# Optimization experiments

Measured on AMD Instinct MI355X. Metric: run time of the kernel, lower is better.

The kernel has to match this reference:

```python
import jax, jax.numpy as jnp
import numpy as np


def setup_inputs() -> dict:
    key = jax.random.key(0)
    k1, k2, k3, k4 = jax.random.split(key, 4)
    B, S, IN, OUT = 4, 2048, 4096, 11008
    input = jax.random.normal(k1, (B, S, IN), dtype=jnp.float32)
    # int8-range quantized weights, stored as int32 (symmetric, zero_point = 0)
    int8_weights = jax.random.randint(k2, (OUT, IN), -128, 128, dtype=jnp.int32)
    scales = jax.random.normal(k3, (OUT,), dtype=jnp.float32)
    bias = jax.random.normal(k4, (1, OUT), dtype=jnp.float32)
    return {"input": input, "int8_weights": int8_weights, "scales": scales, "bias": bias}


def reference(input, int8_weights, scales, bias):
    # w8_a32_forward: dequantize per-output-channel (zero_point = 0) then linear.
    # out = input @ ((q_w * s_w[:, None]).T) + bias
    # Equivalent, cheaper form: scale the GEMM output per column instead of
    # materializing a second fp32 weight copy twice.
    w = int8_weights.astype(jnp.float32)            # [OUT, IN]
    acc = jnp.einsum('bsi,oi->bso', input, w)        # [B, S, OUT]
    return acc * scales + bias                       # broadcast over [B, S, OUT]
```

## Files before the change

kernel.cpp:

```cpp
#include <hip/hip_runtime.h>
#include <hip/hip_bf16.h>
#include <stdint.h>

typedef float f32x4 __attribute__((ext_vector_type(4)));
typedef int i32x4 __attribute__((ext_vector_type(4)));

__device__ __forceinline__ void gload_lds16(const signed char* g, signed char* l) {
    __builtin_amdgcn_global_load_lds(
        (const __attribute__((address_space(1))) unsigned int*)g,
        (__attribute__((address_space(3))) unsigned int*)l,
        16, 0, 0);
}

__global__ __launch_bounds__(256) void quant_rows_kernel(
        const float* __restrict__ A, signed char* __restrict__ Aq,
        float* __restrict__ qrow, int K) {
    const long row = blockIdx.x;
    const float* a = A + row * (long)K;
    signed char* o = Aq + row * (long)K;
    const int tid = threadIdx.x;
    const int nch = K >> 2;
    float amax = 0.f;
    for (int c = tid; c < nch; c += 256) {
        f32x4 v = ((const f32x4*)a)[c];
        amax = fmaxf(amax, fmaxf(fmaxf(fabsf(v[0]), fabsf(v[1])),
                                 fmaxf(fabsf(v[2]), fabsf(v[3]))));
    }
#pragma unroll
    for (int off = 32; off; off >>= 1)
        amax = fmaxf(amax, __shfl_xor(amax, off, 64));
    __shared__ float red[4];
    if ((tid & 63) == 0) red[tid >> 6] = amax;
    __syncthreads();
    amax = fmaxf(fmaxf(red[0], red[1]), fmaxf(red[2], red[3]));
    const float s = amax > 0.f ? 127.f / amax : 0.f;
    if (tid == 0) qrow[row] = amax > 0.f ? amax / 127.f : 0.f;
    for (int c = tid; c < nch; c += 256) {
        f32x4 v = ((const f32x4*)a)[c];
        int r = 0;
#pragma unroll
        for (int i = 0; i < 4; ++i) {
            int q = (int)__builtin_rintf(v[i] * s);
            r |= (q & 0xff) << (8 * i);
        }
        ((int*)o)[c] = r;
    }
}

__global__ __launch_bounds__(256) void cvt_i32_i8_kernel(
        const int* __restrict__ in, signed char* __restrict__ out, long n) {
    long base = ((long)blockIdx.x * 256 + threadIdx.x) * 16;
    long stride = (long)gridDim.x * 256 * 16;
    for (long i = base; i < n; i += stride) {
        i32x4 pk;
#pragma unroll
        for (int c = 0; c < 4; ++c) {
            i32x4 v = *(const i32x4*)(in + i + c * 4);
            pk[c] = (v[0] & 0xff) | ((v[1] & 0xff) << 8) |
                    ((v[2] & 0xff) << 16) | ((v[3] & 0xff) << 24);
        }
        *(i32x4*)(out + i) = pk;
    }
}


template<int BUF, int MH>
__device__ __forceinline__ void readAf(const signed char* smem, i32x4 (&fa)[4],
                                       const int (&off)[4]) {
    const signed char* rg = smem + BUF * 32768 + MH * 8192;
#pragma unroll
    for (int ml = 0; ml < 4; ++ml)
        fa[ml] = *(const i32x4*)(rg + off[ml]);
}

template<int BUF, int NH>
__device__ __forceinline__ void readBf(const signed char* smem, i32x4 (&fb)[2],
                                       const int (&off)[2]) {
    const signed char* rg = smem + BUF * 32768 + 16384 + NH * 8192;
#pragma unroll
    for (int nl = 0; nl < 2; ++nl)
        fb[nl] = *(const i32x4*)(rg + off[nl]);
}

template<int MH, int NH>
__device__ __forceinline__ void mfmas(i32x4 (&acc)[8][4],
                                      const i32x4 (&fa)[4], const i32x4 (&fb)[2]) {
#pragma unroll
    for (int ml = 0; ml < 4; ++ml)
#pragma unroll
        for (int nl = 0; nl < 2; ++nl)
            acc[MH * 4 + ml][NH * 2 + nl] = __builtin_amdgcn_mfma_i32_16x16x64_i8(
                fa[ml], fb[nl], acc[MH * 4 + ml][NH * 2 + nl], 0, 0, 0);
}

#define BARw()  __builtin_amdgcn_s_barrier()
#define LG0()   { asm volatile("s_waitcnt lgkmcnt(0)" ::: "memory"); \
                  __builtin_amdgcn_sched_barrier(0); }
#define P1()    __builtin_amdgcn_s_setprio(1)
#define P0()    __builtin_amdgcn_s_setprio(0)
#define VM2()   asm volatile("s_waitcnt vmcnt(2)" ::: "memory")
#define VM0()   asm volatile("s_waitcnt vmcnt(0)" ::: "memory")

__global__ __launch_bounds__(512, 1) void gemm_i8_8phase(
        const signed char* __restrict__ A,
        const signed char* __restrict__ W,
        const float* __restrict__ qrow,
        const float* __restrict__ scales,
        const float* __restrict__ bias,
        float* __restrict__ C,
        int M, int N, int K) {
    extern __shared__ signed char smem[];

    const int tid  = threadIdx.x;
    const int lane = tid & 63;
    const int wid  = tid >> 6;
    const int wr = wid >> 2;
    const int wc = wid & 3;
    const int fr = lane & 15;
    const int fq = lane >> 4;
    const int kg = lane >> 4;

    const int nwg = gridDim.x;
    const int bid = blockIdx.x;
    const int swz = ((nwg & 7) == 0) ? ((bid & 7) * (nwg >> 3) + (bid >> 3)) : bid;
    const int tiles_n = N >> 8;
    const int tm = swz / tiles_n;
    const int tn = swz % tiles_n;
    const int arow = tm << 8;
    const int brow = tn << 8;

    int aRd[4], bRd[2];
#pragma unroll
    for (int ml = 0; ml < 4; ++ml) {
        const int lrow = wr * 16 + ml * 32 + fr;
        aRd[ml] = lrow * 64 + ((kg ^ ((lrow >> 1) & 3)) << 4);
    }
#pragma unroll
    for (int nl = 0; nl < 2; ++nl) {
        const int lrow = wc * 16 + nl * 64 + fr;
        bRd[nl] = lrow * 64 + ((kg ^ ((lrow >> 1) & 3)) << 4);
    }

    const int srow = tid >> 2;
    const int sswz = (((tid & 3) ^ ((srow >> 1) & 3)) << 4);
    int aOff[2], wOff[2];
#pragma unroll
    for (int h = 0; h < 2; ++h) {
        aOff[h] = (arow + h * 128 + srow) * K + sswz;
        wOff[h] = (brow + h * 128 + srow) * K + sswz;
    }
    const int ldsSt = wid * 1024;

#define STA(kt, h) gload_lds16(A + aOff[h] + (kt) * 64, \
                               smem + ((kt) & 1) * 32768 + (h) * 8192 + ldsSt)
#define STB(kt, h) gload_lds16(W + wOff[h] + (kt) * 64, \
                               smem + ((kt) & 1) * 32768 + 16384 + (h) * 8192 + ldsSt)

    i32x4 acc[8][4] = {};
    i32x4 faA[4], faB[4], fb0[2], fb1[2];

    const int NT = K >> 6;

    STA(0, 0); STB(0, 0); STA(0, 1); STB(0, 1);
    STA(1, 0); STB(1, 0); STB(1, 1);
    asm volatile("s_waitcnt vmcnt(3)" ::: "memory");
    BARw();
    readAf<0, 0>(smem, faA, aRd);
    readBf<0, 0>(smem, fb0, bRd);

    for (int i = 0; i < (NT >> 1) - 1; ++i) {
        const int b = 2 * i + 1, c = 2 * i + 2, d = 2 * i + 3;
        BARw(); LG0(); P1(); mfmas<0, 0>(acc, faA, fb0); P0();
        readBf<0, 1>(smem, fb1, bRd); STA(b, 1);
        BARw(); LG0(); P1(); mfmas<0, 1>(acc, faA, fb1); P0();
        readAf<0, 1>(smem, faB, aRd); STA(c, 0);
        BARw(); LG0(); P1(); mfmas<1, 0>(acc, faB, fb0); P0();
        STB(c, 0); VM2();
        BARw(); P1(); mfmas<1, 1>(acc, faB, fb1); P0();
        readAf<1, 0>(smem, faA, aRd); readBf<1, 0>(smem, fb0, bRd); STB(c, 1);
        BARw(); LG0(); P1(); mfmas<0, 0>(acc, faA, fb0); P0();
        readBf<1, 1>(smem, fb1, bRd); STA(c, 1);
        BARw(); LG0(); P1(); mfmas<0, 1>(acc, faA, fb1); P0();
        readAf<1, 1>(smem, faB, aRd); STA(d, 0);
        BARw(); LG0(); P1(); mfmas<1, 0>(acc, faB, fb0); P0();
        STB(d, 0); VM2();
        BARw(); P1(); mfmas<1, 1>(acc, faB, fb1); P0();
        readAf<0, 0>(smem, faA, aRd); readBf<0, 0>(smem, fb0, bRd); STB(d, 1);
    }

    BARw(); LG0(); P1(); mfmas<0, 0>(acc, faA, fb0); P0();
    readBf<0, 1>(smem, fb1, bRd); STA(NT - 1, 1);
    BARw(); LG0(); P1(); mfmas<0, 1>(acc, faA, fb1); P0();
    readAf<0, 1>(smem, faB, aRd);
    BARw(); LG0(); P1(); mfmas<1, 0>(acc, faB, fb0); P0();
    VM0();
    BARw(); P1(); mfmas<1, 1>(acc, faB, fb1); P0();
    readAf<1, 0>(smem, faA, aRd); readBf<1, 0>(smem, fb0, bRd);
    BARw(); LG0(); P1(); mfmas<0, 0>(acc, faA, fb0); P0();
    readBf<1, 1>(smem, fb1, bRd);
    BARw(); LG0(); P1(); mfmas<0, 1>(acc, faA, fb1); P0();
    readAf<1, 1>(smem, faB, aRd);
    BARw(); LG0(); P1(); mfmas<1, 0>(acc, faB, fb0); P0();
    BARw(); P1(); mfmas<1, 1>(acc, faB, fb1); P0();

#undef STA
#undef STB

    float qr[8][4];
#pragma unroll
    for (int mh = 0; mh < 2; ++mh)
#pragma unroll
        for (int ml = 0; ml < 4; ++ml) {
            const int row0 = arow + wr * 16 + mh * 128 + ml * 32 + fq * 4;
#pragma unroll
            for (int j = 0; j < 4; ++j)
                qr[mh * 4 + ml][j] = qrow[row0 + j];
        }

#pragma unroll
    for (int n = 0; n < 4; ++n) {
        const int col = tn * 256 + wc * 16 + n * 64 + fr;
        const float s = scales[col];
        const float bb = bias[col];
#pragma unroll
        for (int mh = 0; mh < 2; ++mh)
#pragma unroll
            for (int ml = 0; ml < 4; ++ml) {
                const int m = mh * 4 + ml;
                const int row0 = arow + wr * 16 + mh * 128 + ml * 32 + fq * 4;
#pragma unroll
                for (int j = 0; j < 4; ++j)
                    C[(long)(row0 + j) * N + col] =
                        (float)acc[m][n][j] * (qr[m][j] * s) + bb;
            }
    }
}

__global__ __launch_bounds__(256) void gemm_fallback_kernel(
        const float* __restrict__ A, const int* __restrict__ W,
        const float* __restrict__ scales, const float* __restrict__ bias,
        float* __restrict__ C, int M, int N, int K) {
    __shared__ float As[64][16];
    __shared__ float Ws[64][16];
    const int tiles_n = N / 64;
    const int tm = blockIdx.x / tiles_n, tn = blockIdx.x % tiles_n;
    const int tid = threadIdx.x, tx = tid & 15, ty = tid >> 4;
    float acc[4][4] = {};
    for (int k0 = 0; k0 < K; k0 += 16) {
        __syncthreads();
#pragma unroll
        for (int i = 0; i < 4; ++i) {
            const int idx = tid + i * 256;
            const int r = idx >> 4, c = idx & 15;
            As[r][c] = A[(long)(tm * 64 + r) * K + k0 + c];
            Ws[r][c] = (float)W[(long)(tn * 64 + r) * K + k0 + c];
        }
        __syncthreads();
#pragma unroll
        for (int kk = 0; kk < 16; ++kk) {
            float a[4], w[4];
#pragma unroll
            for (int r = 0; r < 4; ++r) a[r] = As[ty * 4 + r][kk];
#pragma unroll
            for (int c = 0; c < 4; ++c) w[c] = Ws[tx * 4 + c][kk];
#pragma unroll
            for (int r = 0; r < 4; ++r)
#pragma unroll
                for (int c = 0; c < 4; ++c) acc[r][c] += a[r] * w[c];
        }
    }
#pragma unroll
    for (int r = 0; r < 4; ++r)
#pragma unroll
        for (int c = 0; c < 4; ++c) {
            const int col = tn * 64 + tx * 4 + c;
            C[(long)(tm * 64 + ty * 4 + r) * N + col] = acc[r][c] * scales[col] + bias[col];
        }
}

extern "C" void kernel_launch(void* const* d_in, const int* in_sizes, int n_in,
                              void* d_out, int out_size, void* d_ws, size_t ws_size,
                              hipStream_t stream) {
    const float* A32    = (const float*)d_in[0];
    const int*   Wq     = (const int*)d_in[1];
    const float* scales = (const float*)d_in[2];
    const float* bias   = (const float*)d_in[3];
    float* C = (float*)d_out;

    const long aElems = in_sizes[0];
    const long wElems = in_sizes[1];
    const int  N = in_sizes[2];
    const int  K = (int)(wElems / N);
    const int  M = (int)(aElems / K);

    const size_t need = (size_t)aElems + (size_t)wElems + (size_t)M * 4 + 64;
    const bool div256 = (M % 256 == 0) && (N % 256 == 0) && (K % 128 == 0) && (K >= 256) &&
                        ((long)M * K < 2000000000L) && ((long)N * K < 2000000000L);

    if (ws_size >= need && div256) {
        signed char* Aq  = (signed char*)d_ws;
        signed char* Wq8 = Aq + aElems;
        float* qrow = (float*)(Wq8 + wElems);
        quant_rows_kernel<<<M, 256, 0, stream>>>(A32, Aq, qrow, K);
        cvt_i32_i8_kernel<<<2048, 256, 0, stream>>>(Wq, Wq8, wElems);
        const int nwg = (M / 256) * (N / 256);
        gemm_i8_8phase<<<nwg, 512, 65536, stream>>>(Aq, Wq8, qrow, scales, bias, C, M, N, K);
    } else {
        const int nwg = (M / 64) * (N / 64);
        gemm_fallback_kernel<<<nwg, 256, 0, stream>>>(A32, Wq, scales, bias, C, M, N, K);
    }
}
```

Before: 482.8 us.

## Restructure int8 GEMM main loop from 8 to 4 phases per K-pair

The int8 MFMA main loop now runs 4 phases per pair of K tiles instead of 8. Each phase issues 16 MFMAs over a full 4x4 fragment block, with all B fragments for a K tile loaded at once into double-buffered register sets. LDS reads and global-to-LDS stores are interleaved before each MFMA cluster behind scheduling barriers. This halves the number of workgroup barriers and waitcnt stalls per tile and gives longer MFMA runs to hide LDS latency, at the cost of more live fragment registers and coarser overlap.

Result: no change. 486.2 us (+0.7%).

```diff
diff --git a/kernel.cpp b/kernel.cpp
--- a/kernel.cpp
+++ b/kernel.cpp
@@ -73,35 +73,40 @@
         fa[ml] = *(const i32x4*)(rg + off[ml]);
 }
 
-template<int BUF, int NH>
-__device__ __forceinline__ void readBf(const signed char* smem, i32x4 (&fb)[2],
-                                       const int (&off)[2]) {
-    const signed char* rg = smem + BUF * 32768 + 16384 + NH * 8192;
-#pragma unroll
-    for (int nl = 0; nl < 2; ++nl)
-        fb[nl] = *(const i32x4*)(rg + off[nl]);
-}
-
-template<int MH, int NH>
-__device__ __forceinline__ void mfmas(i32x4 (&acc)[8][4],
-                                      const i32x4 (&fa)[4], const i32x4 (&fb)[2]) {
+template<int BUF>
+__device__ __forceinline__ void readBf2(const signed char* smem, i32x4 (&fb)[4],
+                                        const int (&off)[2]) {
+#pragma unroll
+    for (int nh = 0; nh < 2; ++nh) {
+        const signed char* rg = smem + BUF * 32768 + 16384 + nh * 8192;
+#pragma unroll
+        for (int nl = 0; nl < 2; ++nl)
+            fb[nh * 2 + nl] = *(const i32x4*)(rg + off[nl]);
+    }
+}
+
+template<int MH>
+__device__ __forceinline__ void mfmas2(i32x4 (&acc)[8][4],
+                                       const i32x4 (&fa)[4], const i32x4 (&fb)[4]) {
 #pragma unroll
     for (int ml = 0; ml < 4; ++ml)
 #pragma unroll
-        for (int nl = 0; nl < 2; ++nl)
-            acc[MH * 4 + ml][NH * 2 + nl] = __builtin_amdgcn_mfma_i32_16x16x64_i8(
-                fa[ml], fb[nl], acc[MH * 4 + ml][NH * 2 + nl], 0, 0, 0);
+        for (int nf = 0; nf < 4; ++nf)
+            acc[MH * 4 + ml][nf] = __builtin_amdgcn_mfma_i32_16x16x64_i8(
+                fa[ml], fb[nf], acc[MH * 4 + ml][nf], 0, 0, 0);
 }
 
 #define BARw()  __builtin_amdgcn_s_barrier()
 #define LG0()   { asm volatile("s_waitcnt lgkmcnt(0)" ::: "memory"); \
                   __builtin_amdgcn_sched_barrier(0); }
+#define SB0()   __builtin_amdgcn_sched_barrier(0)
 #define P1()    __builtin_amdgcn_s_setprio(1)
 #define P0()    __builtin_amdgcn_s_setprio(0)
-#define VM2()   asm volatile("s_waitcnt vmcnt(2)" ::: "memory")
+#define VM1()   asm volatile("s_waitcnt vmcnt(1)" ::: "memory")
+#define VM4()   asm volatile("s_waitcnt vmcnt(4)" ::: "memory")
 #define VM0()   asm volatile("s_waitcnt vmcnt(0)" ::: "memory")
 
-__global__ __launch_bounds__(512, 1) void gemm_i8_8phase(
+__global__ __launch_bounds__(512, 1) void gemm_i8_4phase(
         const signed char* __restrict__ A,
         const signed char* __restrict__ W,
         const float* __restrict__ qrow,
@@ -157,51 +162,54 @@
                                smem + ((kt) & 1) * 32768 + 16384 + (h) * 8192 + ldsSt)
 
     i32x4 acc[8][4] = {};
-    i32x4 faA[4], faB[4], fb0[2], fb1[2];
+    i32x4 aX[4], aY[4], bX[4], bY[4];
 
     const int NT = K >> 6;
 
     STA(0, 0); STB(0, 0); STA(0, 1); STB(0, 1);
-    STA(1, 0); STB(1, 0); STB(1, 1);
-    asm volatile("s_waitcnt vmcnt(3)" ::: "memory");
+    STA(1, 0); STB(1, 0); STA(1, 1); STB(1, 1);
+    VM4();
     BARw();
-    readAf<0, 0>(smem, faA, aRd);
-    readBf<0, 0>(smem, fb0, bRd);
+    readAf<0, 0>(smem, aX, aRd);
+    readBf2<0>(smem, bX, bRd);
 
     for (int i = 0; i < (NT >> 1) - 1; ++i) {
-        const int b = 2 * i + 1, c = 2 * i + 2, d = 2 * i + 3;
-        BARw(); LG0(); P1(); mfmas<0, 0>(acc, faA, fb0); P0();
-        readBf<0, 1>(smem, fb1, bRd); STA(b, 1);
-        BARw(); LG0(); P1(); mfmas<0, 1>(acc, faA, fb1); P0();
-        readAf<0, 1>(smem, faB, aRd); STA(c, 0);
-        BARw(); LG0(); P1(); mfmas<1, 0>(acc, faB, fb0); P0();
-        STB(c, 0); VM2();
-        BARw(); P1(); mfmas<1, 1>(acc, faB, fb1); P0();
-        readAf<1, 0>(smem, faA, aRd); readBf<1, 0>(smem, fb0, bRd); STB(c, 1);
-        BARw(); LG0(); P1(); mfmas<0, 0>(acc, faA, fb0); P0();
-        readBf<1, 1>(smem, fb1, bRd); STA(c, 1);
-        BARw(); LG0(); P1(); mfmas<0, 1>(acc, faA, fb1); P0();
-        readAf<1, 1>(smem, faB, aRd); STA(d, 0);
-        BARw(); LG0(); P1(); mfmas<1, 0>(acc, faB, fb0); P0();
-        STB(d, 0); VM2();
-        BARw(); P1(); mfmas<1, 1>(acc, faB, fb1); P0();
-        readAf<0, 0>(smem, faA, aRd); readBf<0, 0>(smem, fb0, bRd); STB(d, 1);
-    }
-
-    BARw(); LG0(); P1(); mfmas<0, 0>(acc, faA, fb0); P0();
-    readBf<0, 1>(smem, fb1, bRd); STA(NT - 1, 1);
-    BARw(); LG0(); P1(); mfmas<0, 1>(acc, faA, fb1); P0();
-    readAf<0, 1>(smem, faB, aRd);
-    BARw(); LG0(); P1(); mfmas<1, 0>(acc, faB, fb0); P0();
+        const int c = 2 * i + 2, d = 2 * i + 3;
+        BARw(); LG0();
+        readAf<0, 1>(smem, aY, aRd);
+        STA(c, 0); SB0();
+        P1(); mfmas2<0>(acc, aX, bX); P0();
+        VM1();
+        BARw(); LG0();
+        readAf<1, 0>(smem, aX, aRd);
+        readBf2<1>(smem, bY, bRd);
+        STA(c, 1); STB(c, 0); SB0();
+        P1(); mfmas2<1>(acc, aY, bX); P0();
+        BARw(); LG0();
+        readAf<1, 1>(smem, aY, aRd);
+        STB(c, 1); STA(d, 0); SB0();
+        P1(); mfmas2<0>(acc, aX, bY); P0();
+        VM1();
+        BARw(); LG0();
+        readAf<0, 0>(smem, aX, aRd);
+        readBf2<0>(smem, bX, bRd);
+        STA(d, 1); STB(d, 0); STB(d, 1); SB0();
+        P1(); mfmas2<1>(acc, aY, bY); P0();
+    }
+
+    BARw(); LG0();
+    readAf<0, 1>(smem, aY, aRd); SB0();
+    P1(); mfmas2<0>(acc, aX, bX); P0();
     VM0();
-    BARw(); P1(); mfmas<1, 1>(acc, faB, fb1); P0();
-    readAf<1, 0>(smem, faA, aRd); readBf<1, 0>(smem, fb0, bRd);
-    BARw(); LG0(); P1(); mfmas<0, 0>(acc, faA, fb0); P0();
-    readBf<1, 1>(smem, fb1, bRd);
-    BARw(); LG0(); P1(); mfmas<0, 1>(acc, faA, fb1); P0();
-    readAf<1, 1>(smem, faB, aRd);
-    BARw(); LG0(); P1(); mfmas<1, 0>(acc, faB, fb0); P0();
-    BARw(); P1(); mfmas<1, 1>(acc, faB, fb1); P0();
+    BARw(); LG0();
+    readAf<1, 0>(smem, aX, aRd);
+    readBf2<1>(smem, bY, bRd); SB0();
+    P1(); mfmas2<1>(acc, aY, bX); P0();
+    BARw(); LG0();
+    readAf<1, 1>(smem, aY, aRd); SB0();
+    P1(); mfmas2<0>(acc, aX, bY); P0();
+    BARw(); LG0();
+    P1(); mfmas2<1>(acc, aY, bY); P0();
 
 #undef STA
 #undef STB
@@ -304,7 +312,7 @@
         quant_rows_kernel<<<M, 256, 0, stream>>>(A32, Aq, qrow, K);
         cvt_i32_i8_kernel<<<2048, 256, 0, stream>>>(Wq, Wq8, wElems);
         const int nwg = (M / 256) * (N / 256);
-        gemm_i8_8phase<<<nwg, 512, 65536, stream>>>(Aq, Wq8, qrow, scales, bias, C, M, N, K);
+        gemm_i8_4phase<<<nwg, 512, 65536, stream>>>(Aq, Wq8, qrow, scales, bias, C, M, N, K);
     } else {
         const int nwg = (M / 64) * (N / 64);
         gemm_fallback_kernel<<<nwg, 256, 0, stream>>>(A32, Wq, scales, bias, C, M, N, K);
```

## Load A fragments directly to registers and shrink GEMM tile to 128x256

Applied to the files above, without the earlier changes.

Replaces the 256x256 8-phase LDS-staged int8 GEMM with a 128x256 tile in which only W goes through double-buffered LDS. Each wave reads its A fragments straight from global memory into registers. LDS use drops to 32KB and launch bounds allow two workgroups per CU, which aims to raise occupancy and cut LDS traffic and barrier phases. The cost is less A reuse: each wave fetches A directly with narrow 16-byte per-lane loads, and W is re-read by twice as many tiles, which adds global and L2 traffic.

Result: slower. 1.210 ms (+150.6%).

```diff
diff --git a/kernel.cpp b/kernel.cpp
--- a/kernel.cpp
+++ b/kernel.cpp
@@ -64,44 +64,37 @@
 }
 
 
-template<int BUF, int MH>
-__device__ __forceinline__ void readAf(const signed char* smem, i32x4 (&fa)[4],
-                                       const int (&off)[4]) {
-    const signed char* rg = smem + BUF * 32768 + MH * 8192;
-#pragma unroll
-    for (int ml = 0; ml < 4; ++ml)
-        fa[ml] = *(const i32x4*)(rg + off[ml]);
-}
-
-template<int BUF, int NH>
-__device__ __forceinline__ void readBf(const signed char* smem, i32x4 (&fb)[2],
-                                       const int (&off)[2]) {
-    const signed char* rg = smem + BUF * 32768 + 16384 + NH * 8192;
-#pragma unroll
-    for (int nl = 0; nl < 2; ++nl)
-        fb[nl] = *(const i32x4*)(rg + off[nl]);
-}
-
-template<int MH, int NH>
-__device__ __forceinline__ void mfmas(i32x4 (&acc)[8][4],
-                                      const i32x4 (&fa)[4], const i32x4 (&fb)[2]) {
-#pragma unroll
-    for (int ml = 0; ml < 4; ++ml)
-#pragma unroll
-        for (int nl = 0; nl < 2; ++nl)
-            acc[MH * 4 + ml][NH * 2 + nl] = __builtin_amdgcn_mfma_i32_16x16x64_i8(
-                fa[ml], fb[nl], acc[MH * 4 + ml][NH * 2 + nl], 0, 0, 0);
-}
-
-#define BARw()  __builtin_amdgcn_s_barrier()
-#define LG0()   { asm volatile("s_waitcnt lgkmcnt(0)" ::: "memory"); \
-                  __builtin_amdgcn_sched_barrier(0); }
-#define P1()    __builtin_amdgcn_s_setprio(1)
-#define P0()    __builtin_amdgcn_s_setprio(0)
-#define VM2()   asm volatile("s_waitcnt vmcnt(2)" ::: "memory")
-#define VM0()   asm volatile("s_waitcnt vmcnt(0)" ::: "memory")
-
-__global__ __launch_bounds__(512, 1) void gemm_i8_8phase(
+#define PHASE(T, BUF, DOSTAGE, VMST, VMA)                                    \
+  {                                                                          \
+    __builtin_amdgcn_s_barrier();                                            \
+    __builtin_amdgcn_sched_barrier(0);                                       \
+    if (DOSTAGE) {                                                           \
+      gload_lds16(W + wOff0 + ((T) + 1) * 64,                                \
+                  smem + (1 - (BUF)) * 16384 + ldsSt);                       \
+      gload_lds16(W + wOff1 + ((T) + 1) * 64,                                \
+                  smem + (1 - (BUF)) * 16384 + 8192 + ldsSt);                \
+    }                                                                        \
+    _Pragma("unroll")                                                        \
+    for (int ml = 0; ml < 4; ++ml)                                           \
+      fa[ml] = *(const i32x4*)(A + aAddr[ml] + (T) * 64);                    \
+    asm volatile("s_waitcnt vmcnt(" #VMST ")" ::: "memory");                 \
+    __builtin_amdgcn_s_barrier();                                            \
+    __builtin_amdgcn_sched_barrier(0);                                       \
+    _Pragma("unroll")                                                        \
+    for (int nl = 0; nl < 4; ++nl)                                           \
+      fb[nl] = *(const i32x4*)(smem + (BUF) * 16384 + bRd[nl]);              \
+    asm volatile("s_waitcnt vmcnt(" #VMA ")" ::: "memory");                  \
+    __builtin_amdgcn_s_setprio(1);                                           \
+    _Pragma("unroll")                                                        \
+    for (int ml = 0; ml < 4; ++ml)                                           \
+      _Pragma("unroll")                                                      \
+      for (int nl = 0; nl < 4; ++nl)                                         \
+        acc[ml][nl] = __builtin_amdgcn_mfma_i32_16x16x64_i8(                 \
+            fa[ml], fb[nl], acc[ml][nl], 0, 0, 0);                           \
+    __builtin_amdgcn_s_setprio(0);                                           \
+  }
+
+__global__ __launch_bounds__(512, 2) void gemm_i8_areg(
         const signed char* __restrict__ A,
         const signed char* __restrict__ W,
         const float* __restrict__ qrow,
@@ -117,7 +110,6 @@
     const int wr = wid >> 2;
     const int wc = wid & 3;
     const int fr = lane & 15;
-    const int fq = lane >> 4;
     const int kg = lane >> 4;
 
     const int nwg = gridDim.x;
@@ -126,113 +118,65 @@
     const int tiles_n = N >> 8;
     const int tm = swz / tiles_n;
     const int tn = swz % tiles_n;
-    const int arow = tm << 8;
+    const int arow = tm << 7;
     const int brow = tn << 8;
 
-    int aRd[4], bRd[2];
+    int aAddr[4];
+#pragma unroll
+    for (int ml = 0; ml < 4; ++ml)
+        aAddr[ml] = (arow + wr * 64 + ml * 16 + fr) * K + kg * 16;
+
+    const int srow = tid >> 2;
+    const int sswz = ((tid & 3) ^ ((srow >> 1) & 3)) << 4;
+    const int wOff0 = (brow + srow) * K + sswz;
+    const int wOff1 = (brow + 128 + srow) * K + sswz;
+    const int ldsSt = wid * 1024;
+
+    int bRd[4];
+#pragma unroll
+    for (int nl = 0; nl < 4; ++nl) {
+        const int lrow = wc * 64 + nl * 16 + fr;
+        bRd[nl] = lrow * 64 + ((kg ^ ((lrow >> 1) & 3)) << 4);
+    }
+
+    i32x4 acc[4][4] = {};
+    i32x4 fa[4], fb[4];
+
+    const int NT = K >> 6;
+
+    gload_lds16(W + wOff0, smem + ldsSt);
+    gload_lds16(W + wOff1, smem + 8192 + ldsSt);
+
+    for (int i = 0; i < (NT >> 1) - 1; ++i) {
+        const int t0 = 2 * i;
+        PHASE(t0,     0, true, 6, 2);
+        PHASE(t0 + 1, 1, true, 6, 2);
+    }
+    PHASE(NT - 2, 0, true,  6, 2);
+    PHASE(NT - 1, 1, false, 4, 0);
+
+    float qr[4][4];
 #pragma unroll
     for (int ml = 0; ml < 4; ++ml) {
-        const int lrow = wr * 16 + ml * 32 + fr;
-        aRd[ml] = lrow * 64 + ((kg ^ ((lrow >> 1) & 3)) << 4);
-    }
-#pragma unroll
-    for (int nl = 0; nl < 2; ++nl) {
-        const int lrow = wc * 16 + nl * 64 + fr;
-        bRd[nl] = lrow * 64 + ((kg ^ ((lrow >> 1) & 3)) << 4);
-    }
-
-    const int srow = tid >> 2;
-    const int sswz = (((tid & 3) ^ ((srow >> 1) & 3)) << 4);
-    int aOff[2], wOff[2];
-#pragma unroll
-    for (int h = 0; h < 2; ++h) {
-        aOff[h] = (arow + h * 128 + srow) * K + sswz;
-        wOff[h] = (brow + h * 128 + srow) * K + sswz;
-    }
-    const int ldsSt = wid * 1024;
-
-#define STA(kt, h) gload_lds16(A + aOff[h] + (kt) * 64, \
-                               smem + ((kt) & 1) * 32768 + (h) * 8192 + ldsSt)
-#define STB(kt, h) gload_lds16(W + wOff[h] + (kt) * 64, \
-                               smem + ((kt) & 1) * 32768 + 16384 + (h) * 8192 + ldsSt)
-
-    i32x4 acc[8][4] = {};
-    i32x4 faA[4], faB[4], fb0[2], fb1[2];
-
-    const int NT = K >> 6;
-
-    STA(0, 0); STB(0, 0); STA(0, 1); STB(0, 1);
-    STA(1, 0); STB(1, 0); STB(1, 1);
-    asm volatile("s_waitcnt vmcnt(3)" ::: "memory");
-    BARw();
-    readAf<0, 0>(smem, faA, aRd);
-    readBf<0, 0>(smem, fb0, bRd);
-
-    for (int i = 0; i < (NT >> 1) - 1; ++i) {
-        const int b = 2 * i + 1, c = 2 * i + 2, d = 2 * i + 3;
-        BARw(); LG0(); P1(); mfmas<0, 0>(acc, faA, fb0); P0();
-        readBf<0, 1>(smem, fb1, bRd); STA(b, 1);
-        BARw(); LG0(); P1(); mfmas<0, 1>(acc, faA, fb1); P0();
-        readAf<0, 1>(smem, faB, aRd); STA(c, 0);
-        BARw(); LG0(); P1(); mfmas<1, 0>(acc, faB, fb0); P0();
-        STB(c, 0); VM2();
-        BARw(); P1(); mfmas<1, 1>(acc, faB, fb1); P0();
-        readAf<1, 0>(smem, faA, aRd); readBf<1, 0>(smem, fb0, bRd); STB(c, 1);
-        BARw(); LG0(); P1(); mfmas<0, 0>(acc, faA, fb0); P0();
-        readBf<1, 1>(smem, fb1, bRd); STA(c, 1);
-        BARw(); LG0(); P1(); mfmas<0, 1>(acc, faA, fb1); P0();
-        readAf<1, 1>(smem, faB, aRd); STA(d, 0);
-        BARw(); LG0(); P1(); mfmas<1, 0>(acc, faB, fb0); P0();
-        STB(d, 0); VM2();
-        BARw(); P1(); mfmas<1, 1>(acc, faB, fb1); P0();
-        readAf<0, 0>(smem, faA, aRd); readBf<0, 0>(smem, fb0, bRd); STB(d, 1);
-    }
-
-    BARw(); LG0(); P1(); mfmas<0, 0>(acc, faA, fb0); P0();
-    readBf<0, 1>(smem, fb1, bRd); STA(NT - 1, 1);
-    BARw(); LG0(); P1(); mfmas<0, 1>(acc, faA, fb1); P0();
-    readAf<0, 1>(smem, faB, aRd);
-    BARw(); LG0(); P1(); mfmas<1, 0>(acc, faB, fb0); P0();
-    VM0();
-    BARw(); P1(); mfmas<1, 1>(acc, faB, fb1); P0();
-    readAf<1, 0>(smem, faA, aRd); readBf<1, 0>(smem, fb0, bRd);
-    BARw(); LG0(); P1(); mfmas<0, 0>(acc, faA, fb0); P0();
-    readBf<1, 1>(smem, fb1, bRd);
-    BARw(); LG0(); P1(); mfmas<0, 1>(acc, faA, fb1); P0();
-    readAf<1, 1>(smem, faB, aRd);
-    BARw(); LG0(); P1(); mfmas<1, 0>(acc, faB, fb0); P0();
-    BARw(); P1(); mfmas<1, 1>(acc, faB, fb1); P0();
-
-#undef STA
-#undef STB
-
-    float qr[8][4];
-#pragma unroll
-    for (int mh = 0; mh < 2; ++mh)
-#pragma unroll
-        for (int ml = 0; ml < 4; ++ml) {
-            const int row0 = arow + wr * 16 + mh * 128 + ml * 32 + fq * 4;
-#pragma unroll
-            for (int j = 0; j < 4; ++j)
-                qr[mh * 4 + ml][j] = qrow[row0 + j];
-        }
-
-#pragma unroll
-    for (int n = 0; n < 4; ++n) {
-        const int col = tn * 256 + wc * 16 + n * 64 + fr;
+        const int row0 = arow + wr * 64 + ml * 16 + kg * 4;
+#pragma unroll
+        for (int j = 0; j < 4; ++j)
+            qr[ml][j] = qrow[row0 + j];
+    }
+
+#pragma unroll
+    for (int nl = 0; nl < 4; ++nl) {
+        const int col = tn * 256 + wc * 64 + nl * 16 + fr;
         const float s = scales[col];
         const float bb = bias[col];
 #pragma unroll
-        for (int mh = 0; mh < 2; ++mh)
-#pragma unroll
-            for (int ml = 0; ml < 4; ++ml) {
-                const int m = mh * 4 + ml;
-                const int row0 = arow + wr * 16 + mh * 128 + ml * 32 + fq * 4;
-#pragma unroll
-                for (int j = 0; j < 4; ++j)
-                    C[(long)(row0 + j) * N + col] =
-                        (float)acc[m][n][j] * (qr[m][j] * s) + bb;
-            }
+        for (int ml = 0; ml < 4; ++ml) {
+            const int row0 = arow + wr * 64 + ml * 16 + kg * 4;
+#pragma unroll
+            for (int j = 0; j < 4; ++j)
+                C[(long)(row0 + j) * N + col] =
+                    (float)acc[ml][nl][j] * (qr[ml][j] * s) + bb;
+        }
     }
 }
 
@@ -294,17 +238,17 @@
     const int  M = (int)(aElems / K);
 
     const size_t need = (size_t)aElems + (size_t)wElems + (size_t)M * 4 + 64;
-    const bool div256 = (M % 256 == 0) && (N % 256 == 0) && (K % 128 == 0) && (K >= 256) &&
-                        ((long)M * K < 2000000000L) && ((long)N * K < 2000000000L);
-
-    if (ws_size >= need && div256) {
+    const bool ok = (M % 128 == 0) && (N % 256 == 0) && (K % 128 == 0) && (K >= 128) &&
+                    ((long)M * K < 2000000000L) && ((long)N * K < 2000000000L);
+
+    if (ws_size >= need && ok) {
         signed char* Aq  = (signed char*)d_ws;
         signed char* Wq8 = Aq + aElems;
         float* qrow = (float*)(Wq8 + wElems);
         quant_rows_kernel<<<M, 256, 0, stream>>>(A32, Aq, qrow, K);
         cvt_i32_i8_kernel<<<2048, 256, 0, stream>>>(Wq, Wq8, wElems);
-        const int nwg = (M / 256) * (N / 256);
-        gemm_i8_8phase<<<nwg, 512, 65536, stream>>>(Aq, Wq8, qrow, scales, bias, C, M, N, K);
+        const int nwg = (M / 128) * (N / 256);
+        gemm_i8_areg<<<nwg, 512, 32768, stream>>>(Aq, Wq8, qrow, scales, bias, C, M, N, K);
     } else {
         const int nwg = (M / 64) * (N / 64);
         gemm_fallback_kernel<<<nwg, 256, 0, stream>>>(A32, Wq, scales, bias, C, M, N, K);
```

## Load weight fragments directly into registers, staging only activations through LDS

Applied to the files above, without the earlier changes.

The int8 GEMM no longer stages weight tiles through shared memory. Each wave now loads its B fragments straight from global memory into registers, two k-tiles ahead. Only activation tiles are double-buffered in LDS, which halves the LDS footprint to 32 KB and cuts the pipeline to a simpler 4-phase schedule with adjusted vmcnt waits. The aim is to remove LDS write/read traffic and barrier pressure for B. The cost is that waves sharing the same columns fetch identical weight data redundantly from cache, and global load latency is exposed more directly.

Measured after the change: 660.7 us. +36.8%, slower.

```diff
diff --git a/kernel.cpp b/kernel.cpp
--- a/kernel.cpp
+++ b/kernel.cpp
@@ -67,41 +67,51 @@
 template<int BUF, int MH>
 __device__ __forceinline__ void readAf(const signed char* smem, i32x4 (&fa)[4],
                                        const int (&off)[4]) {
-    const signed char* rg = smem + BUF * 32768 + MH * 8192;
+    const signed char* rg = smem + BUF * 16384 + MH * 8192;
 #pragma unroll
     for (int ml = 0; ml < 4; ++ml)
         fa[ml] = *(const i32x4*)(rg + off[ml]);
-}
-
-template<int BUF, int NH>
-__device__ __forceinline__ void readBf(const signed char* smem, i32x4 (&fb)[2],
-                                       const int (&off)[2]) {
-    const signed char* rg = smem + BUF * 32768 + 16384 + NH * 8192;
-#pragma unroll
-    for (int nl = 0; nl < 2; ++nl)
-        fb[nl] = *(const i32x4*)(rg + off[nl]);
-}
-
-template<int MH, int NH>
-__device__ __forceinline__ void mfmas(i32x4 (&acc)[8][4],
-                                      const i32x4 (&fa)[4], const i32x4 (&fb)[2]) {
-#pragma unroll
-    for (int ml = 0; ml < 4; ++ml)
-#pragma unroll
-        for (int nl = 0; nl < 2; ++nl)
-            acc[MH * 4 + ml][NH * 2 + nl] = __builtin_amdgcn_mfma_i32_16x16x64_i8(
-                fa[ml], fb[nl], acc[MH * 4 + ml][NH * 2 + nl], 0, 0, 0);
 }
 
 #define BARw()  __builtin_amdgcn_s_barrier()
 #define LG0()   { asm volatile("s_waitcnt lgkmcnt(0)" ::: "memory"); \
                   __builtin_amdgcn_sched_barrier(0); }
+#define SB0()   __builtin_amdgcn_sched_barrier(0)
 #define P1()    __builtin_amdgcn_s_setprio(1)
 #define P0()    __builtin_amdgcn_s_setprio(0)
-#define VM2()   asm volatile("s_waitcnt vmcnt(2)" ::: "memory")
-#define VM0()   asm volatile("s_waitcnt vmcnt(0)" ::: "memory")
-
-__global__ __launch_bounds__(512, 1) void gemm_i8_8phase(
+#define VM4()   asm volatile("s_waitcnt vmcnt(4)" ::: "memory")
+#define VM8()   asm volatile("s_waitcnt vmcnt(8)" ::: "memory")
+
+#define MFMAS(MH, FA, FB)                                                     \
+  _Pragma("unroll")                                                           \
+  for (int ml = 0; ml < 4; ++ml)                                              \
+    _Pragma("unroll")                                                         \
+    for (int nf = 0; nf < 4; ++nf)                                            \
+      acc[(MH) * 4 + ml][nf] = __builtin_amdgcn_mfma_i32_16x16x64_i8(         \
+          FA[ml], FB[nf], acc[(MH) * 4 + ml][nf], 0, 0, 0);
+
+#define LOADB(T, FB)                                                          \
+  _Pragma("unroll")                                                           \
+  for (int nf = 0; nf < 4; ++nf)                                              \
+    FB[nf] = *(const i32x4*)(W + bGOff[nf] + (T) * 64);
+
+#define STAGEA(T, P) {                                                        \
+    gload_lds16(A + aOff0 + (T) * 64, smem + (P) * 16384 + ldsSt);            \
+    gload_lds16(A + aOff1 + (T) * 64, smem + (P) * 16384 + 8192 + ldsSt); }
+
+#define PH1(P, FB) {                                                          \
+    BARw(); LG0();                                                            \
+    readAf<P, 1>(smem, faB, aRd); SB0();                                      \
+    P1(); MFMAS(0, faA, FB); P0(); }
+
+#define PH2_FULL(T, P, FB) {                                                  \
+    VM4(); BARw(); LG0();                                                     \
+    readAf<(P) ^ 1, 0>(smem, faA, aRd);                                       \
+    STAGEA((T) + 2, P); SB0();                                                \
+    P1(); MFMAS(1, faB, FB); P0();                                            \
+    LOADB((T) + 2, FB); }
+
+__global__ __launch_bounds__(512, 1) void gemm_i8_breg(
         const signed char* __restrict__ A,
         const signed char* __restrict__ W,
         const float* __restrict__ qrow,
@@ -129,82 +139,55 @@
     const int arow = tm << 8;
     const int brow = tn << 8;
 
-    int aRd[4], bRd[2];
+    int aRd[4];
 #pragma unroll
     for (int ml = 0; ml < 4; ++ml) {
         const int lrow = wr * 16 + ml * 32 + fr;
         aRd[ml] = lrow * 64 + ((kg ^ ((lrow >> 1) & 3)) << 4);
     }
-#pragma unroll
-    for (int nl = 0; nl < 2; ++nl) {
-        const int lrow = wc * 16 + nl * 64 + fr;
-        bRd[nl] = lrow * 64 + ((kg ^ ((lrow >> 1) & 3)) << 4);
-    }
 
     const int srow = tid >> 2;
-    const int sswz = (((tid & 3) ^ ((srow >> 1) & 3)) << 4);
-    int aOff[2], wOff[2];
-#pragma unroll
-    for (int h = 0; h < 2; ++h) {
-        aOff[h] = (arow + h * 128 + srow) * K + sswz;
-        wOff[h] = (brow + h * 128 + srow) * K + sswz;
-    }
+    const int sswz = ((tid & 3) ^ ((srow >> 1) & 3)) << 4;
+    const int aOff0 = (arow + srow) * K + sswz;
+    const int aOff1 = (arow + 128 + srow) * K + sswz;
     const int ldsSt = wid * 1024;
 
-#define STA(kt, h) gload_lds16(A + aOff[h] + (kt) * 64, \
-                               smem + ((kt) & 1) * 32768 + (h) * 8192 + ldsSt)
-#define STB(kt, h) gload_lds16(W + wOff[h] + (kt) * 64, \
-                               smem + ((kt) & 1) * 32768 + 16384 + (h) * 8192 + ldsSt)
+    int bGOff[4];
+#pragma unroll
+    for (int nf = 0; nf < 4; ++nf)
+        bGOff[nf] = (brow + nf * 64 + wc * 16 + fr) * K + kg * 16;
 
     i32x4 acc[8][4] = {};
-    i32x4 faA[4], faB[4], fb0[2], fb1[2];
+    i32x4 faA[4], faB[4], fbX[4], fbY[4];
 
     const int NT = K >> 6;
 
-    STA(0, 0); STB(0, 0); STA(0, 1); STB(0, 1);
-    STA(1, 0); STB(1, 0); STB(1, 1);
-    asm volatile("s_waitcnt vmcnt(3)" ::: "memory");
+    STAGEA(0, 0);
+    STAGEA(1, 1);
+    LOADB(0, fbX);
+    LOADB(1, fbY);
+    VM8();
     BARw();
     readAf<0, 0>(smem, faA, aRd);
-    readBf<0, 0>(smem, fb0, bRd);
 
     for (int i = 0; i < (NT >> 1) - 1; ++i) {
-        const int b = 2 * i + 1, c = 2 * i + 2, d = 2 * i + 3;
-        BARw(); LG0(); P1(); mfmas<0, 0>(acc, faA, fb0); P0();
-        readBf<0, 1>(smem, fb1, bRd); STA(b, 1);
-        BARw(); LG0(); P1(); mfmas<0, 1>(acc, faA, fb1); P0();
-        readAf<0, 1>(smem, faB, aRd); STA(c, 0);
-        BARw(); LG0(); P1(); mfmas<1, 0>(acc, faB, fb0); P0();
-        STB(c, 0); VM2();
-        BARw(); P1(); mfmas<1, 1>(acc, faB, fb1); P0();
-        readAf<1, 0>(smem, faA, aRd); readBf<1, 0>(smem, fb0, bRd); STB(c, 1);
-        BARw(); LG0(); P1(); mfmas<0, 0>(acc, faA, fb0); P0();
-        readBf<1, 1>(smem, fb1, bRd); STA(c, 1);
-        BARw(); LG0(); P1(); mfmas<0, 1>(acc, faA, fb1); P0();
-        readAf<1, 1>(smem, faB, aRd); STA(d, 0);
-        BARw(); LG0(); P1(); mfmas<1, 0>(acc, faB, fb0); P0();
-        STB(d, 0); VM2();
-        BARw(); P1(); mfmas<1, 1>(acc, faB, fb1); P0();
-        readAf<0, 0>(smem, faA, aRd); readBf<0, 0>(smem, fb0, bRd); STB(d, 1);
-    }
-
-    BARw(); LG0(); P1(); mfmas<0, 0>(acc, faA, fb0); P0();
-    readBf<0, 1>(smem, fb1, bRd); STA(NT - 1, 1);
-    BARw(); LG0(); P1(); mfmas<0, 1>(acc, faA, fb1); P0();
-    readAf<0, 1>(smem, faB, aRd);
-    BARw(); LG0(); P1(); mfmas<1, 0>(acc, faB, fb0); P0();
-    VM0();
-    BARw(); P1(); mfmas<1, 1>(acc, faB, fb1); P0();
-    readAf<1, 0>(smem, faA, aRd); readBf<1, 0>(smem, fb0, bRd);
-    BARw(); LG0(); P1(); mfmas<0, 0>(acc, faA, fb0); P0();
-    readBf<1, 1>(smem, fb1, bRd);
-    BARw(); LG0(); P1(); mfmas<0, 1>(acc, faA, fb1); P0();
-    readAf<1, 1>(smem, faB, aRd);
-    BARw(); LG0(); P1(); mfmas<1, 0>(acc, faB, fb0); P0();
-    BARw(); P1(); mfmas<1, 1>(acc, faB, fb1); P0();
-
-#undef STA
-#undef STB
+        const int t0 = 2 * i;
+        PH1(0, fbX);
+        PH2_FULL(t0, 0, fbX);
+        PH1(1, fbY);
+        PH2_FULL(t0 + 1, 1, fbY);
+    }
+
+    PH1(0, fbX);
+    {
+        VM4(); BARw(); LG0();
+        readAf<1, 0>(smem, faA, aRd);
+        SB0();
+        P1(); MFMAS(1, faB, fbX); P0();
+    }
+    PH1(1, fbY);
+    LG0();
+    P1(); MFMAS(1, faB, fbY); P0();
 
     float qr[8][4];
 #pragma unroll
@@ -294,17 +277,17 @@
     const int  M = (int)(aElems / K);
 
     const size_t need = (size_t)aElems + (size_t)wElems + (size_t)M * 4 + 64;
-    const bool div256 = (M % 256 == 0) && (N % 256 == 0) && (K % 128 == 0) && (K >= 256) &&
-                        ((long)M * K < 2000000000L) && ((long)N * K < 2000000000L);
-
-    if (ws_size >= need && div256) {
+    const bool ok = (M % 256 == 0) && (N % 256 == 0) && (K % 128 == 0) && (K >= 256) &&
+                    ((long)M * K < 2000000000L) && ((long)N * K < 2000000000L);
+
+    if (ws_size >= need && ok) {
         signed char* Aq  = (signed char*)d_ws;
         signed char* Wq8 = Aq + aElems;
         float* qrow = (float*)(Wq8 + wElems);
         quant_rows_kernel<<<M, 256, 0, stream>>>(A32, Aq, qrow, K);
         cvt_i32_i8_kernel<<<2048, 256, 0, stream>>>(Wq, Wq8, wElems);
         const int nwg = (M / 256) * (N / 256);
-        gemm_i8_8phase<<<nwg, 512, 65536, stream>>>(Aq, Wq8, qrow, scales, bias, C, M, N, K);
+        gemm_i8_breg<<<nwg, 512, 32768, stream>>>(Aq, Wq8, qrow, scales, bias, C, M, N, K);
     } else {
         const int nwg = (M / 64) * (N / 64);
         gemm_fallback_kernel<<<nwg, 256, 0, stream>>>(A32, Wq, scales, bias, C, M, N, K);
```
